# Performance work log

Measured on AMD Instinct MI355X. Metric: run time of the kernel, lower is better.

## Reference

```python
import jax, jax.numpy as jnp
import numpy as np

N = 100000   # nodes per type
E = 800000   # edges per relation
D = 128      # hidden/out channels


def _sage(x_src, x_dst, src, dst, Wl, bl, Wr, n_dst):
    # PyG SAGEConv (mean aggr, bipartite): lin_l(mean_j x_src[j]) + lin_r(x_dst)
    msg = x_src[src]                                                    # [E, D] gather
    agg = jax.ops.segment_sum(msg, dst, num_segments=n_dst)            # [n_dst, D]
    cnt = jax.ops.segment_sum(jnp.ones((src.shape[0],), x_src.dtype), dst, num_segments=n_dst)
    mean = agg / jnp.maximum(cnt, 1.0)[:, None]
    return mean @ Wl.T + bl + x_dst @ Wr.T


def _metapath(xu, xi, ei0, ei1, Wl0, bl0, Wr0, Wl1, bl1, Wr1, outW, outb):
    # hop0: user -> item ; hop1: item -> user ; start_type = 'user'
    hi = jax.nn.relu(_sage(xu, xi, ei0[0], ei0[1], Wl0, bl0, Wr0, xi.shape[0]))
    hu = jax.nn.relu(_sage(hi, xu, ei1[0], ei1[1], Wl1, bl1, Wr1, xu.shape[0]))
    return hu @ outW.T + outb                                           # [N, D]


def setup_inputs() -> dict:
    key = jax.random.key(0)
    ks = jax.random.split(key, 32)
    s = 1.0 / np.sqrt(D)
    w = lambda k, shp: (jax.random.normal(k, shp, jnp.float32) * s)
    d = {
        'x_user': jax.random.normal(ks[0], (N, D), jnp.float32),
        'x_item': jax.random.normal(ks[1], (N, D), jnp.float32),
        'ei_m0_h0': jax.random.randint(ks[2], (2, E), 0, N),
        'ei_m0_h1': jax.random.randint(ks[3], (2, E), 0, N),
        'ei_m1_h0': jax.random.randint(ks[4], (2, E), 0, N),
        'ei_m1_h1': jax.random.randint(ks[5], (2, E), 0, N),
    }
    names = ['Wl_00', 'Wr_00', 'Wl_01', 'Wr_01', 'Wl_10', 'Wr_10', 'Wl_11', 'Wr_11', 'outW_0', 'outW_1']
    for i, nm in enumerate(names):
        d[nm] = w(ks[6 + i], (D, D))
    for nm in ['bl_00', 'bl_01', 'bl_10', 'bl_11', 'outb_0', 'outb_1']:
        d[nm] = jnp.zeros((D,), jnp.float32)
    d['regW'] = w(ks[20], (1, 2 * D))
    d['regb'] = jnp.zeros((1,), jnp.float32)
    return d


def reference(x_user, x_item, ei_m0_h0, ei_m0_h1, ei_m1_h0, ei_m1_h1,
              Wl_00, bl_00, Wr_00, Wl_01, bl_01, Wr_01,
              Wl_10, bl_10, Wr_10, Wl_11, bl_11, Wr_11,
              outW_0, outb_0, outW_1, outb_1, regW, regb):
    emb0 = _metapath(x_user, x_item, ei_m0_h0, ei_m0_h1,
                     Wl_00, bl_00, Wr_00, Wl_01, bl_01, Wr_01, outW_0, outb_0)
    emb1 = _metapath(x_user, x_item, ei_m1_h0, ei_m1_h1,
                     Wl_10, bl_10, Wr_10, Wl_11, bl_11, Wr_11, outW_1, outb_1)
    concat = jnp.concatenate([emb0, emb1], axis=-1)                     # [N, 2D]
    return (concat @ regW.T + regb).squeeze(-1)                         # [N]
```

## Files before the change

kernel.cpp:

```cpp
#include <hip/hip_runtime.h>

#define DIM 128
#define CHUNK 8192
#define PAIRC 4096
#define SENT 0xFFFFFFFFu
#define STAGECAP 14080
typedef unsigned short ushort_t;
typedef short bf16x8 __attribute__((ext_vector_type(8)));
typedef float f32x4 __attribute__((ext_vector_type(4)));

__device__ inline ushort_t f2bf(float f) {
    unsigned int u = __float_as_uint(f);
    unsigned int r = (u + 0x7FFFu + ((u >> 16) & 1u)) >> 16;
    return (ushort_t)r;
}
__device__ inline unsigned int pack2bf(float lo, float hi) {
    return (unsigned int)f2bf(lo) | ((unsigned int)f2bf(hi) << 16);
}
__device__ inline float bflo2f(unsigned int u) { return __uint_as_float(u << 16); }
__device__ inline float bfhi2f(unsigned int u) { return __uint_as_float(u & 0xFFFF0000u); }

__global__ void f32_to_bf16_2_kernel(const float* __restrict__ a, const float* __restrict__ b,
                                     ushort_t* __restrict__ oa, ushort_t* __restrict__ ob, int n4) {
    const float* __restrict__ in = blockIdx.y ? b : a;
    ushort_t* __restrict__ out = blockIdx.y ? ob : oa;
    int i = blockIdx.x * blockDim.x + threadIdx.x;
    int stride = gridDim.x * blockDim.x;
    for (; i < n4; i += stride) {
        float4 v = *reinterpret_cast<const float4*>(in + (size_t)i * 4);
        ushort_t o[4] = {f2bf(v.x), f2bf(v.y), f2bf(v.z), f2bf(v.w)};
        *reinterpret_cast<uint2*>(out + (size_t)i * 4) = *reinterpret_cast<uint2*>(o);
    }
}

struct WPack { const float* Wl[4]; const float* Wr[4]; };

__global__ void pack_weights4_kernel(WPack wp, ushort_t* __restrict__ Wcat) {
    int l = blockIdx.y, j = blockIdx.x, k = threadIdx.x;
    float v = (k < DIM) ? wp.Wl[l][j * DIM + k] : wp.Wr[l][j * DIM + (k - DIM)];
    Wcat[l * 32768 + j * 256 + k] = f2bf(v);
}

__global__ void precompute_v_kernel(const float* __restrict__ outW0,
                                    const float* __restrict__ outW1,
                                    const float* __restrict__ outb0,
                                    const float* __restrict__ outb1,
                                    const float* __restrict__ regW,
                                    const float* __restrict__ regb,
                                    float* __restrict__ vbuf) {
    int t = threadIdx.x;
    if (t < DIM) {
        float s = 0.f;
        #pragma unroll 8
        for (int j = 0; j < DIM; ++j) s = fmaf(outW0[j * DIM + t], regW[j], s);
        vbuf[t] = s;
    } else {
        int k = t - DIM;
        float s = 0.f;
        #pragma unroll 8
        for (int j = 0; j < DIM; ++j) s = fmaf(outW1[j * DIM + k], regW[DIM + j], s);
        vbuf[t] = s;
    }
    if (t == 0) {
        float c = regb[0];
        for (int j = 0; j < DIM; ++j) c += outb0[j] * regW[j] + outb1[j] * regW[DIM + j];
        vbuf[2 * DIM] = c;
    }
}

struct EdgePtrs { const int* e[4]; };

__global__ void bin4_stage_kernel(EdgePtrs eps, int nedges, int* __restrict__ bpad,
                                  int* __restrict__ breal,
                                  unsigned int* __restrict__ pairs, int nbuck) {
    int list = blockIdx.y;
    const int* __restrict__ src = eps.e[list];
    const int* __restrict__ dst = eps.e[list] + nedges;
    __shared__ int cnt[512], loff[512], goff[512];
    __shared__ int wsum[4];
    __shared__ unsigned int stage[STAGECAP];
    const int tid = threadIdx.x;
    const int lane = tid & 63, w = tid >> 6;
    const int base = blockIdx.x * CHUNK;

    for (int b = tid; b < 512; b += 256) cnt[b] = 0;
    __syncthreads();

    int dstv[CHUNK / 256];
    #pragma unroll
    for (int it = 0; it < CHUNK / 256; ++it) {
        int e = base + it * 256 + tid;
        int d = (e < nedges) ? dst[e] : -1;
        dstv[it] = d;
        if (d >= 0) atomicAdd(&cnt[d >> 8], 1);
    }
    __syncthreads();

    {
        int b0 = tid * 2, b1 = b0 + 1;
        int r0 = (cnt[b0] + 15) & ~15;
        int r1 = (cnt[b1] + 15) & ~15;
        int s = r0 + r1;
        int sv = s;
        #pragma unroll
        for (int off = 1; off < 64; off <<= 1) {
            int u = __shfl_up(sv, off);
            if (lane >= off) sv += u;
        }
        if (lane == 63) wsum[w] = sv;
        __syncthreads();
        int bw = 0;
        #pragma unroll
        for (int k = 0; k < 4; ++k)
            if (k < w) bw += wsum[k];
        int ex = bw + sv - s;
        loff[b0] = ex;
        loff[b1] = ex + r0;
    }
    for (int b = tid; b < nbuck; b += 256) {
        int c = cnt[b];
        int res = (c + 15) & ~15;
        if (res > 0) {
            goff[b] = atomicAdd(&bpad[list * nbuck + b], res);
            atomicAdd(&breal[list * nbuck + b], c);
        }
        cnt[b] = 0;
    }
    __syncthreads();

    #pragma unroll
    for (int it = 0; it < CHUNK / 256; ++it) {
        int d = dstv[it];
        if (d >= 0) {
            int e = base + it * 256 + tid;
            int r = atomicAdd(&cnt[d >> 8], 1);
            stage[loff[d >> 8] + r] = ((unsigned int)src[e] << 8) | (unsigned int)(d & 255);
        }
    }
    __syncthreads();

    for (int b = w; b < nbuck; b += 4) {
        int c = cnt[b];
        int res = (c + 15) & ~15;
        if (res == 0) continue;
        size_t go = ((size_t)list * nbuck + b) * PAIRC + goff[b];
        int lo = loff[b];
        for (int i = lane; i < res; i += 64)
            pairs[go + i] = (i < c) ? stage[lo + i] : SENT;
    }
}

__global__ void bucket_scan_kernel(const int* __restrict__ breal, int* __restrict__ bbase,
                                   int n, int* __restrict__ rowptr, int n4, int total) {
    int t = threadIdx.x;
    int loc[4];
    int s = 0;
    #pragma unroll
    for (int k = 0; k < 4; ++k) {
        int i = t * 4 + k;
        loc[k] = (i < n) ? breal[i] : 0;
        s += loc[k];
    }
    int lane = t & 63, w = t >> 6;
    int sv = s;
    #pragma unroll
    for (int off = 1; off < 64; off <<= 1) {
        int u = __shfl_up(sv, off);
        if (lane >= off) sv += u;
    }
    __shared__ int wsum[8];
    if (lane == 63) wsum[w] = sv;
    __syncthreads();
    int base = 0;
    #pragma unroll
    for (int k = 0; k < 8; ++k)
        if (k < w) base += wsum[k];
    int ex = base + sv - s;
    #pragma unroll
    for (int k = 0; k < 4; ++k) {
        int i = t * 4 + k;
        if (i < n) bbase[i] = ex;
        ex += loc[k];
    }
    if (t == 0) rowptr[n4] = total;
}

__global__ void fillb_kernel(const unsigned int* __restrict__ pairs, const int* __restrict__ bpad,
                             const int* __restrict__ bbase, int* __restrict__ rowptr,
                             int* __restrict__ eidx, int N, int nbuck) {
    int list = blockIdx.y;
    int b = blockIdx.x;
    int d0 = b << 8;
    if (d0 >= N) return;
    int nd = N - d0; if (nd > 256) nd = 256;
    int slot = list * nbuck + b;
    int cntp = bpad[slot];
    int base = bbase[slot];
    const unsigned int* __restrict__ ps = pairs + (size_t)slot * PAIRC;

    __shared__ int h[256], cur[256];
    int t = threadIdx.x;
    h[t] = 0;
    __syncthreads();
    for (int i = t; i < cntp; i += 256) {
        unsigned int p = ps[i];
        if (p != SENT) atomicAdd(&h[p & 255u], 1);
    }
    __syncthreads();
    int v = h[t];
    int lane = t & 63, w = t >> 6;
    int sv = v;
    #pragma unroll
    for (int off = 1; off < 64; off <<= 1) {
        int u = __shfl_up(sv, off);
        if (lane >= off) sv += u;
    }
    __shared__ int wsum[4];
    if (lane == 63) wsum[w] = sv;
    __syncthreads();
    int wbase = 0;
    #pragma unroll
    for (int k = 0; k < 4; ++k)
        if (k < w) wbase += wsum[k];
    int ex = wbase + sv - v;
    if (t < nd) rowptr[(size_t)list * N + d0 + t] = base + ex;
    cur[t] = ex;
    __syncthreads();
    for (int i = t; i < cntp; i += 256) {
        unsigned int p = ps[i];
        if (p != SENT) {
            int ld = (int)(p & 255u);
            int r = atomicAdd(&cur[ld], 1);
            eidx[base + r] = (int)(p >> 8);
        }
    }
}

__global__ void aggregate_kernel(const ushort_t* __restrict__ xsrc,
                                 const int* __restrict__ rowptr,
                                 const int* __restrict__ eidx,
                                 ushort_t* __restrict__ mean, int n) {
    int wid = (blockIdx.x * blockDim.x + threadIdx.x) >> 6;
    int lane = threadIdx.x & 63;
    int nw = (gridDim.x * blockDim.x) >> 6;
    const int sub = lane >> 4;
    const int lr = lane & 15;
    for (int r = wid; r < n; r += nw) {
        int beg = rowptr[r];
        int end = rowptr[r + 1];
        int deg = end - beg;
        float a[8] = {0.f, 0.f, 0.f, 0.f, 0.f, 0.f, 0.f, 0.f};
        int nit = (deg + 3) >> 2;
        for (int it = 0; it < nit; ++it) {
            int j = beg + it * 4 + sub;
            if (j < end) {
                int s = eidx[j];
                uint4 u = *reinterpret_cast<const uint4*>(xsrc + (size_t)s * DIM + lr * 8);
                a[0] += bflo2f(u.x); a[1] += bfhi2f(u.x);
                a[2] += bflo2f(u.y); a[3] += bfhi2f(u.y);
                a[4] += bflo2f(u.z); a[5] += bfhi2f(u.z);
                a[6] += bflo2f(u.w); a[7] += bfhi2f(u.w);
            }
        }
        #pragma unroll
        for (int k = 0; k < 8; ++k) {
            a[k] += __shfl_xor(a[k], 16);
            a[k] += __shfl_xor(a[k], 32);
        }
        if (sub == 0) {
            float sc = 1.0f / fmaxf((float)deg, 1.0f);
            uint4 o;
            o.x = pack2bf(a[0] * sc, a[1] * sc);
            o.y = pack2bf(a[2] * sc, a[3] * sc);
            o.z = pack2bf(a[4] * sc, a[5] * sc);
            o.w = pack2bf(a[6] * sc, a[7] * sc);
            *reinterpret_cast<uint4*>(mean + (size_t)r * DIM + lr * 8) = o;
        }
    }
}

template <int MODE>
__launch_bounds__(256, 2)
__global__ void sage_gemm_mfma(const ushort_t* __restrict__ A0,
                               const ushort_t* __restrict__ A1,
                               const ushort_t* __restrict__ Wcat,
                               const float* __restrict__ bl,
                               ushort_t* __restrict__ H,
                               const float* __restrict__ v,
                               const float* __restrict__ cptr,
                               float* __restrict__ out,
                               int nrows) {
    __shared__ ushort_t As[128][40];
    __shared__ ushort_t Bs[128][40];
    __shared__ float red[2][128];

    const int tid = threadIdx.x;
    const int lane = tid & 63;
    const int w = tid >> 6;
    const int wr = w >> 1, wc = w & 1;
    const int lr = lane & 15;
    const int lk = (lane >> 4) * 8;
    const int row0 = blockIdx.x * 128;

    f32x4 acc[4][4];
    #pragma unroll
    for (int m = 0; m < 4; ++m)
        #pragma unroll
        for (int n = 0; n < 4; ++n)
            acc[m][n] = (f32x4){0.f, 0.f, 0.f, 0.f};

    for (int kt = 0; kt < 8; ++kt) {
        const int kb = kt * 32;
        const ushort_t* __restrict__ Asrc = (kb < DIM) ? A0 : A1;
        const int kbb = kb & (DIM - 1);

        #pragma unroll
        for (int p = 0; p < 2; ++p) {
            int idx = p * 256 + tid;
            int r = idx >> 2, c = idx & 3;
            int grow = row0 + r;
            uint4 val = make_uint4(0u, 0u, 0u, 0u);
            if (grow < nrows)
                val = *reinterpret_cast<const uint4*>(Asrc + (size_t)grow * DIM + kbb + c * 8);
            *reinterpret_cast<uint4*>(&As[r][c * 8]) = val;
        }
        #pragma unroll
        for (int p = 0; p < 2; ++p) {
            int idx = p * 256 + tid;
            int j = idx >> 2, c = idx & 3;
            uint4 val = *reinterpret_cast<const uint4*>(Wcat + j * 256 + kb + c * 8);
            *reinterpret_cast<uint4*>(&Bs[j][c * 8]) = val;
        }
        __syncthreads();

        bf16x8 af[4], bfm[4];
        #pragma unroll
        for (int m = 0; m < 4; ++m)
            af[m] = *reinterpret_cast<const bf16x8*>(&As[wr * 64 + m * 16 + lr][lk]);
        #pragma unroll
        for (int n = 0; n < 4; ++n)
            bfm[n] = *reinterpret_cast<const bf16x8*>(&Bs[wc * 64 + n * 16 + lr][lk]);
        #pragma unroll
        for (int m = 0; m < 4; ++m)
            #pragma unroll
            for (int n = 0; n < 4; ++n)
                acc[m][n] = __builtin_amdgcn_mfma_f32_16x16x32_bf16(af[m], bfm[n], acc[m][n], 0, 0, 0);
        __syncthreads();
    }

    if (MODE == 0) {
        float blc[4];
        #pragma unroll
        for (int n = 0; n < 4; ++n) blc[n] = bl[wc * 64 + n * 16 + lr];
        #pragma unroll
        for (int m = 0; m < 4; ++m) {
            #pragma unroll
            for (int reg = 0; reg < 4; ++reg) {
                int row = row0 + wr * 64 + m * 16 + (lane >> 4) * 4 + reg;
                if (row < nrows) {
                    #pragma unroll
                    for (int n = 0; n < 4; ++n) {
                        int col = wc * 64 + n * 16 + lr;
                        H[(size_t)row * DIM + col] = f2bf(fmaxf(acc[m][n][reg] + blc[n], 0.f));
                    }
                }
            }
        }
    } else {
        float blc[4], vc[4];
        #pragma unroll
        for (int n = 0; n < 4; ++n) {
            int col = wc * 64 + n * 16 + lr;
            blc[n] = bl[col];
            vc[n] = v[col];
        }
        #pragma unroll
        for (int m = 0; m < 4; ++m) {
            float rp[4] = {0.f, 0.f, 0.f, 0.f};
            #pragma unroll
            for (int n = 0; n < 4; ++n)
                #pragma unroll
                for (int reg = 0; reg < 4; ++reg)
                    rp[reg] = fmaf(fmaxf(acc[m][n][reg] + blc[n], 0.f), vc[n], rp[reg]);
            #pragma unroll
            for (int reg = 0; reg < 4; ++reg) {
                float p = rp[reg];
                p += __shfl_xor(p, 1);
                p += __shfl_xor(p, 2);
                p += __shfl_xor(p, 4);
                p += __shfl_xor(p, 8);
                if (lr == 0)
                    red[wc][wr * 64 + m * 16 + (lane >> 4) * 4 + reg] = p;
            }
        }
        __syncthreads();
        if (tid < 128) {
            int row = row0 + tid;
            if (row < nrows) {
                float s = red[0][tid] + red[1][tid];
                if (MODE == 1) out[row] = cptr[0] + s;
                else out[row] += s;
            }
        }
    }
}

extern "C" void kernel_launch(void* const* d_in, const int* in_sizes, int n_in,
                              void* d_out, int out_size, void* d_ws, size_t ws_size,
                              hipStream_t stream) {
    const float* x_user = (const float*)d_in[0];
    const float* x_item = (const float*)d_in[1];
    const int* ei_m0_h0 = (const int*)d_in[2];
    const int* ei_m0_h1 = (const int*)d_in[3];
    const int* ei_m1_h0 = (const int*)d_in[4];
    const int* ei_m1_h1 = (const int*)d_in[5];
    const float* Wl00 = (const float*)d_in[6];
    const float* Wr00 = (const float*)d_in[7];
    const float* Wl01 = (const float*)d_in[8];
    const float* Wr01 = (const float*)d_in[9];
    const float* Wl10 = (const float*)d_in[10];
    const float* Wr10 = (const float*)d_in[11];
    const float* Wl11 = (const float*)d_in[12];
    const float* Wr11 = (const float*)d_in[13];
    const float* outW0 = (const float*)d_in[14];
    const float* outW1 = (const float*)d_in[15];
    const float* bl00 = (const float*)d_in[16];
    const float* bl01 = (const float*)d_in[17];
    const float* bl10 = (const float*)d_in[18];
    const float* bl11 = (const float*)d_in[19];
    const float* outb0 = (const float*)d_in[20];
    const float* outb1 = (const float*)d_in[21];
    const float* regW = (const float*)d_in[22];
    const float* regb = (const float*)d_in[23];

    const int N = in_sizes[0] / DIM;
    const int E = in_sizes[2] / 2;
    float* out = (float*)d_out;

    const int n4 = 4 * N;
    const int nbuck = (N + 255) >> 8;
    ushort_t* xbu = (ushort_t*)d_ws;
    ushort_t* xbi = xbu + (size_t)N * DIM;
    ushort_t* meanb = xbi + (size_t)N * DIM;
    ushort_t* hib = meanb + (size_t)N * DIM;
    unsigned int* pairs = (unsigned int*)meanb;
    ushort_t* Wcat = hib + (size_t)N * DIM;
    float* vbuf = (float*)(Wcat + 4 * 128 * 256);
    int* bpad = (int*)(vbuf + 2 * DIM + 1);
    int* breal = bpad + 4 * nbuck;
    int* bbase = breal + 4 * nbuck;
    int* rowptr = bbase + 4 * nbuck;
    int* eidx = rowptr + n4 + 1;

    f32_to_bf16_2_kernel<<<dim3(1024, 2), 256, 0, stream>>>(x_user, x_item, xbu, xbi, N * DIM / 4);
    WPack wp;
    wp.Wl[0] = Wl00; wp.Wl[1] = Wl01; wp.Wl[2] = Wl10; wp.Wl[3] = Wl11;
    wp.Wr[0] = Wr00; wp.Wr[1] = Wr01; wp.Wr[2] = Wr10; wp.Wr[3] = Wr11;
    pack_weights4_kernel<<<dim3(128, 4), 256, 0, stream>>>(wp, Wcat);
    precompute_v_kernel<<<1, 256, 0, stream>>>(outW0, outW1, outb0, outb1, regW, regb, vbuf);

    EdgePtrs eps;
    eps.e[0] = ei_m0_h0; eps.e[1] = ei_m0_h1; eps.e[2] = ei_m1_h0; eps.e[3] = ei_m1_h1;
    hipMemsetAsync(bpad, 0, (size_t)8 * nbuck * sizeof(int), stream);
    bin4_stage_kernel<<<dim3((E + CHUNK - 1) / CHUNK, 4), 256, 0, stream>>>(eps, E, bpad, breal, pairs, nbuck);
    bucket_scan_kernel<<<1, 512, 0, stream>>>(breal, bbase, 4 * nbuck, rowptr, n4, 4 * E);
    fillb_kernel<<<dim3(nbuck, 4), 256, 0, stream>>>(pairs, bpad, bbase, rowptr, eidx, N, nbuck);

    const int gemmBlocks = (N + 127) / 128;
    const int aggBlocks = 2048;

    struct Hop {
        const ushort_t* xsrc;
        const ushort_t* xdst;
        const ushort_t* W;
        const float* bl;
        int mode;
        const float* v;
    };
    const Hop hops[4] = {
        {xbu, xbi, Wcat + 0 * 32768, bl00, 0, nullptr},
        {hib, xbu, Wcat + 1 * 32768, bl01, 1, vbuf},
        {xbu, xbi, Wcat + 2 * 32768, bl10, 0, nullptr},
        {hib, xbu, Wcat + 3 * 32768, bl11, 2, vbuf + DIM},
    };

    for (int h = 0; h < 4; ++h) {
        const Hop& hp = hops[h];
        aggregate_kernel<<<aggBlocks, 256, 0, stream>>>(hp.xsrc, rowptr + (size_t)h * N, eidx, meanb, N);
        if (hp.mode == 0)
            sage_gemm_mfma<0><<<gemmBlocks, 256, 0, stream>>>(meanb, hp.xdst, hp.W, hp.bl,
                                                              hib, nullptr, nullptr, nullptr, N);
        else if (hp.mode == 1)
            sage_gemm_mfma<1><<<gemmBlocks, 256, 0, stream>>>(meanb, hp.xdst, hp.W, hp.bl,
                                                              nullptr, hp.v, vbuf + 2 * DIM, out, N);
        else
            sage_gemm_mfma<2><<<gemmBlocks, 256, 0, stream>>>(meanb, hp.xdst, hp.W, hp.bl,
                                                              nullptr, hp.v, vbuf + 2 * DIM, out, N);
    }
}
```

Before: 373.2 us.

## Fuse neighbor mean aggregation into SAGE MFMA GEMM via shared memory

Removes the separate aggregate kernel. Each GEMM block now gathers and averages neighbor rows for its 128 destination rows straight into a shared-memory tile, and the first half of the K loop reads from that tile. This avoids writing the mean buffer to global memory and reading it back, and saves four kernel launches. The cost is a larger shared-memory footprint, lower occupancy during the latency-bound gather, and one wave walking 32 rows serially. The edge-binning chunk and stage-capacity constants are also reduced, and the workspace layout is repacked so the pair buffer aliases the hidden buffer.

```diff
diff --git a/kernel.cpp b/kernel.cpp
--- a/kernel.cpp
+++ b/kernel.cpp
@@ -1,10 +1,10 @@
 #include <hip/hip_runtime.h>
 
 #define DIM 128
-#define CHUNK 8192
+#define CHUNK 4096
 #define PAIRC 4096
 #define SENT 0xFFFFFFFFu
-#define STAGECAP 14080
+#define STAGECAP 9984
 typedef unsigned short ushort_t;
 typedef short bf16x8 __attribute__((ext_vector_type(8)));
 typedef float f32x4 __attribute__((ext_vector_type(4)));
@@ -236,60 +236,20 @@
     }
 }
 
-__global__ void aggregate_kernel(const ushort_t* __restrict__ xsrc,
-                                 const int* __restrict__ rowptr,
-                                 const int* __restrict__ eidx,
-                                 ushort_t* __restrict__ mean, int n) {
-    int wid = (blockIdx.x * blockDim.x + threadIdx.x) >> 6;
-    int lane = threadIdx.x & 63;
-    int nw = (gridDim.x * blockDim.x) >> 6;
-    const int sub = lane >> 4;
-    const int lr = lane & 15;
-    for (int r = wid; r < n; r += nw) {
-        int beg = rowptr[r];
-        int end = rowptr[r + 1];
-        int deg = end - beg;
-        float a[8] = {0.f, 0.f, 0.f, 0.f, 0.f, 0.f, 0.f, 0.f};
-        int nit = (deg + 3) >> 2;
-        for (int it = 0; it < nit; ++it) {
-            int j = beg + it * 4 + sub;
-            if (j < end) {
-                int s = eidx[j];
-                uint4 u = *reinterpret_cast<const uint4*>(xsrc + (size_t)s * DIM + lr * 8);
-                a[0] += bflo2f(u.x); a[1] += bfhi2f(u.x);
-                a[2] += bflo2f(u.y); a[3] += bfhi2f(u.y);
-                a[4] += bflo2f(u.z); a[5] += bfhi2f(u.z);
-                a[6] += bflo2f(u.w); a[7] += bfhi2f(u.w);
-            }
-        }
-        #pragma unroll
-        for (int k = 0; k < 8; ++k) {
-            a[k] += __shfl_xor(a[k], 16);
-            a[k] += __shfl_xor(a[k], 32);
-        }
-        if (sub == 0) {
-            float sc = 1.0f / fmaxf((float)deg, 1.0f);
-            uint4 o;
-            o.x = pack2bf(a[0] * sc, a[1] * sc);
-            o.y = pack2bf(a[2] * sc, a[3] * sc);
-            o.z = pack2bf(a[4] * sc, a[5] * sc);
-            o.w = pack2bf(a[6] * sc, a[7] * sc);
-            *reinterpret_cast<uint4*>(mean + (size_t)r * DIM + lr * 8) = o;
-        }
-    }
-}
-
 template <int MODE>
 __launch_bounds__(256, 2)
-__global__ void sage_gemm_mfma(const ushort_t* __restrict__ A0,
-                               const ushort_t* __restrict__ A1,
-                               const ushort_t* __restrict__ Wcat,
-                               const float* __restrict__ bl,
-                               ushort_t* __restrict__ H,
-                               const float* __restrict__ v,
-                               const float* __restrict__ cptr,
-                               float* __restrict__ out,
-                               int nrows) {
+__global__ void sage_fused(const ushort_t* __restrict__ xsrc,
+                           const ushort_t* __restrict__ xdst,
+                           const int* __restrict__ rowptr,
+                           const int* __restrict__ eidx,
+                           const ushort_t* __restrict__ Wcat,
+                           const float* __restrict__ bl,
+                           ushort_t* __restrict__ H,
+                           const float* __restrict__ v,
+                           const float* __restrict__ cptr,
+                           float* __restrict__ out,
+                           int nrows) {
+    __shared__ ushort_t Am[128][136];
     __shared__ ushort_t As[128][40];
     __shared__ ushort_t Bs[128][40];
     __shared__ float red[2][128];
@@ -302,6 +262,53 @@
     const int lk = (lane >> 4) * 8;
     const int row0 = blockIdx.x * 128;
 
+    {
+        const int sub = lane >> 4;
+        int rpv = 0;
+        {
+            int ridx = row0 + w * 32 + lane;
+            if (lane <= 32) rpv = rowptr[ridx <= nrows ? ridx : nrows];
+        }
+        for (int i = 0; i < 32; ++i) {
+            int rl = w * 32 + i;
+            int r = row0 + rl;
+            int beg = __shfl(rpv, i);
+            int end = __shfl(rpv, i + 1);
+            float a[8] = {0.f, 0.f, 0.f, 0.f, 0.f, 0.f, 0.f, 0.f};
+            int deg = 0;
+            if (r < nrows) {
+                deg = end - beg;
+                int nit = (deg + 3) >> 2;
+                for (int it = 0; it < nit; ++it) {
+                    int j = beg + it * 4 + sub;
+                    if (j < end) {
+                        int s = eidx[j];
+                        uint4 u = *reinterpret_cast<const uint4*>(xsrc + (size_t)s * DIM + lr * 8);
+                        a[0] += bflo2f(u.x); a[1] += bfhi2f(u.x);
+                        a[2] += bflo2f(u.y); a[3] += bfhi2f(u.y);
+                        a[4] += bflo2f(u.z); a[5] += bfhi2f(u.z);
+                        a[6] += bflo2f(u.w); a[7] += bfhi2f(u.w);
+                    }
+                }
+            }
+            #pragma unroll
+            for (int k = 0; k < 8; ++k) {
+                a[k] += __shfl_xor(a[k], 16);
+                a[k] += __shfl_xor(a[k], 32);
+            }
+            if (sub == 0) {
+                float sc = 1.0f / fmaxf((float)deg, 1.0f);
+                uint4 o;
+                o.x = pack2bf(a[0] * sc, a[1] * sc);
+                o.y = pack2bf(a[2] * sc, a[3] * sc);
+                o.z = pack2bf(a[4] * sc, a[5] * sc);
+                o.w = pack2bf(a[6] * sc, a[7] * sc);
+                *reinterpret_cast<uint4*>(&Am[rl][lr * 8]) = o;
+            }
+        }
+    }
+    __syncthreads();
+
     f32x4 acc[4][4];
     #pragma unroll
     for (int m = 0; m < 4; ++m)
@@ -311,18 +318,20 @@
 
     for (int kt = 0; kt < 8; ++kt) {
         const int kb = kt * 32;
-        const ushort_t* __restrict__ Asrc = (kb < DIM) ? A0 : A1;
+        const bool fromLds = (kt < 4);
         const int kbb = kb & (DIM - 1);
 
-        #pragma unroll
-        for (int p = 0; p < 2; ++p) {
-            int idx = p * 256 + tid;
-            int r = idx >> 2, c = idx & 3;
-            int grow = row0 + r;
-            uint4 val = make_uint4(0u, 0u, 0u, 0u);
-            if (grow < nrows)
-                val = *reinterpret_cast<const uint4*>(Asrc + (size_t)grow * DIM + kbb + c * 8);
-            *reinterpret_cast<uint4*>(&As[r][c * 8]) = val;
+        if (!fromLds) {
+            #pragma unroll
+            for (int p = 0; p < 2; ++p) {
+                int idx = p * 256 + tid;
+                int r = idx >> 2, c = idx & 3;
+                int grow = row0 + r;
+                uint4 val = make_uint4(0u, 0u, 0u, 0u);
+                if (grow < nrows)
+                    val = *reinterpret_cast<const uint4*>(xdst + (size_t)grow * DIM + kbb + c * 8);
+                *reinterpret_cast<uint4*>(&As[r][c * 8]) = val;
+            }
         }
         #pragma unroll
         for (int p = 0; p < 2; ++p) {
@@ -335,8 +344,11 @@
 
         bf16x8 af[4], bfm[4];
         #pragma unroll
-        for (int m = 0; m < 4; ++m)
-            af[m] = *reinterpret_cast<const bf16x8*>(&As[wr * 64 + m * 16 + lr][lk]);
+        for (int m = 0; m < 4; ++m) {
+            int row = wr * 64 + m * 16 + lr;
+            af[m] = fromLds ? *reinterpret_cast<const bf16x8*>(&Am[row][kbb + lk])
+                            : *reinterpret_cast<const bf16x8*>(&As[row][lk]);
+        }
         #pragma unroll
         for (int n = 0; n < 4; ++n)
             bfm[n] = *reinterpret_cast<const bf16x8*>(&Bs[wc * 64 + n * 16 + lr][lk]);
@@ -439,13 +451,15 @@
 
     const int n4 = 4 * N;
     const int nbuck = (N + 255) >> 8;
+    const size_t hibElems = (size_t)N * DIM;
+    const size_t pairElems = (size_t)4 * nbuck * PAIRC;
+    const size_t regionShorts = (pairElems * 2 > hibElems) ? pairElems * 2 : hibElems;
     ushort_t* xbu = (ushort_t*)d_ws;
-    ushort_t* xbi = xbu + (size_t)N * DIM;
-    ushort_t* meanb = xbi + (size_t)N * DIM;
-    ushort_t* hib = meanb + (size_t)N * DIM;
-    unsigned int* pairs = (unsigned int*)meanb;
-    ushort_t* Wcat = hib + (size_t)N * DIM;
-    float* vbuf = (float*)(Wcat + 4 * 128 * 256);
+    ushort_t* xbi = xbu + hibElems;
+    ushort_t* hib = xbi + hibElems;
+    unsigned int* pairs = (unsigned int*)hib;
+    ushort_t* Wcat = hib + regionShorts;
+    float* vbuf = (float*)(Wcat + 4 * 32768);
     int* bpad = (int*)(vbuf + 2 * DIM + 1);
     int* breal = bpad + 4 * nbuck;
     int* bbase = breal + 4 * nbuck;
@@ -467,7 +481,6 @@
     fillb_kernel<<<dim3(nbuck, 4), 256, 0, stream>>>(pairs, bpad, bbase, rowptr, eidx, N, nbuck);
 
     const int gemmBlocks = (N + 127) / 128;
-    const int aggBlocks = 2048;
 
     struct Hop {
         const ushort_t* xsrc;
@@ -486,15 +499,15 @@
 
     for (int h = 0; h < 4; ++h) {
         const Hop& hp = hops[h];
-        aggregate_kernel<<<aggBlocks, 256, 0, stream>>>(hp.xsrc, rowptr + (size_t)h * N, eidx, meanb, N);
+        const int* rp = rowptr + (size_t)h * N;
         if (hp.mode == 0)
-            sage_gemm_mfma<0><<<gemmBlocks, 256, 0, stream>>>(meanb, hp.xdst, hp.W, hp.bl,
-                                                              hib, nullptr, nullptr, nullptr, N);
+            sage_fused<0><<<gemmBlocks, 256, 0, stream>>>(hp.xsrc, hp.xdst, rp, eidx, hp.W, hp.bl,
+                                                          hib, nullptr, nullptr, nullptr, N);
         else if (hp.mode == 1)
-            sage_gemm_mfma<1><<<gemmBlocks, 256, 0, stream>>>(meanb, hp.xdst, hp.W, hp.bl,
-                                                              nullptr, hp.v, vbuf + 2 * DIM, out, N);
+            sage_fused<1><<<gemmBlocks, 256, 0, stream>>>(hp.xsrc, hp.xdst, rp, eidx, hp.W, hp.bl,
+                                                          nullptr, hp.v, vbuf + 2 * DIM, out, N);
         else
-            sage_gemm_mfma<2><<<gemmBlocks, 256, 0, stream>>>(meanb, hp.xdst, hp.W, hp.bl,
-                                                              nullptr, hp.v, vbuf + 2 * DIM, out, N);
-    }
-}
+            sage_fused<2><<<gemmBlocks, 256, 0, stream>>>(hp.xsrc, hp.xdst, rp, eidx, hp.W, hp.bl,
+                                                          nullptr, hp.v, vbuf + 2 * DIM, out, N);
+    }
+}
```

New measurement: 709.2 us. 90.0% more time.
